# Kernel optimization log

Measured on AMD Instinct MI355X. Metric: run time of the kernel, lower is better.

Reference implementation:

```python
import jax, jax.numpy as jnp
import numpy as np

N = 50000      # nodes
E = 800000     # edges (no self loops; GATConv adds them itself)
F_IN = 128     # in_channels
ED = 16        # edge_attr_dim
H1, C1 = 8, 8  # layer-1 heads/channels -> 64 concat
OUT = 128      # out_channels
G = 256        # graphs in batch
NEG_SLOPE = 0.2


def setup_inputs() -> dict:
    key = jax.random.key(0)
    ks = jax.random.split(key, 20)
    x = jax.random.normal(ks[0], (N, F_IN), jnp.float32)
    src = jax.random.randint(ks[1], (E,), 0, N, jnp.int32)
    off = jax.random.randint(ks[2], (E,), 1, N, jnp.int32)
    dst = ((src + off) % N).astype(jnp.int32)  # guaranteed no self loops
    edge_index = jnp.stack([src, dst])
    edge_attr = jax.random.normal(ks[3], (E, ED), jnp.float32)
    batch = jnp.sort(jax.random.randint(ks[4], (N,), 0, G, jnp.int32))
    def glorot(k, shape, fan_in):
        return jax.random.normal(k, shape, jnp.float32) / np.sqrt(fan_in)
    params = dict(
        W1=glorot(ks[5], (F_IN, H1 * C1), F_IN),
        att_src1=glorot(ks[6], (H1, C1), C1),
        att_dst1=glorot(ks[7], (H1, C1), C1),
        att_edge1=glorot(ks[8], (H1, C1), C1),
        We1=glorot(ks[9], (ED, H1 * C1), ED),
        b1=jnp.zeros((H1 * C1,), jnp.float32),
        W2=glorot(ks[10], (H1 * C1, OUT), H1 * C1),
        att_src2=glorot(ks[11], (1, OUT), OUT),
        att_dst2=glorot(ks[12], (1, OUT), OUT),
        att_edge2=glorot(ks[13], (1, OUT), OUT),
        We2=glorot(ks[14], (ED, OUT), ED),
        b2=jnp.zeros((OUT,), jnp.float32),
    )
    return dict(x=x, edge_index=edge_index, edge_attr=edge_attr, batch=batch, **params)


def _segment_softmax(a, seg, n):
    m = jax.ops.segment_max(a, seg, num_segments=n)
    e = jnp.exp(a - m[seg])
    s = jax.ops.segment_sum(e, seg, num_segments=n)
    return e / (s[seg] + 1e-16)


def _gat_layer(x, src, dst, ea_full, W, a_s, a_d, a_e, We, b, heads, ch, concat):
    n = x.shape[0]
    xw = (x @ W).reshape(n, heads, ch)                       # [N,H,C]
    al_s = jnp.einsum('nhc,hc->nh', xw, a_s)                  # [N,H]
    al_d = jnp.einsum('nhc,hc->nh', xw, a_d)
    ew = (ea_full @ We).reshape(-1, heads, ch)                # [E',H,C]
    al_e = jnp.einsum('ehc,hc->eh', ew, a_e)
    alpha = al_s[src] + al_d[dst] + al_e                      # [E',H]
    alpha = jax.nn.leaky_relu(alpha, NEG_SLOPE)
    alpha = _segment_softmax(alpha, dst, n)                   # softmax over incoming edges
    out = jax.ops.segment_sum(xw[src] * alpha[:, :, None], dst, num_segments=n)
    out = out.reshape(n, heads * ch) if concat else out.mean(axis=1)
    return out + b


def reference(x, edge_index, edge_attr, batch,
              W1, att_src1, att_dst1, att_edge1, We1, b1,
              W2, att_src2, att_dst2, att_edge2, We2, b2):
    src, dst = edge_index[0], edge_index[1]
    n = x.shape[0]
    # add self loops; self-loop edge_attr = mean of incoming edge_attr (fill_value='mean')
    ones = jnp.ones((src.shape[0],), x.dtype)
    deg = jax.ops.segment_sum(ones, dst, num_segments=n)
    ea_self = jax.ops.segment_sum(edge_attr, dst, num_segments=n) / jnp.maximum(deg, 1.0)[:, None]
    loop = jnp.arange(n, dtype=src.dtype)
    src_f = jnp.concatenate([src, loop])
    dst_f = jnp.concatenate([dst, loop])
    ea_full = jnp.concatenate([edge_attr, ea_self], axis=0)

    h = _gat_layer(x, src_f, dst_f, ea_full, W1, att_src1, att_dst1, att_edge1, We1, b1, H1, C1, True)
    h = jax.nn.elu(h)
    h = _gat_layer(h, src_f, dst_f, ea_full, W2, att_src2, att_dst2, att_edge2, We2, b2, 1, OUT, True)

    # global mean pool over graphs
    cnt = jax.ops.segment_sum(jnp.ones((n,), h.dtype), batch, num_segments=G)
    pooled = jax.ops.segment_sum(h, batch, num_segments=G) / jnp.maximum(cnt, 1.0)[:, None]
    return pooled
```

## Files before the change

### kernel.cpp

```cpp
#include <hip/hip_runtime.h>
#include <hip/hip_bf16.h>
#include <math.h>

#define N_NODES 50000
#define N_EDGES 800000
#define F_IN    128
#define ED_DIM  16
#define D1      64
#define NGRAPH  256
#define OUT_C   128

__global__ void prep_kernel(const float* __restrict__ W1, const float* __restrict__ W2,
                            float* __restrict__ W1t, float* __restrict__ W2t) {
  int t = blockIdx.x * 256 + threadIdx.x;
  if (t < 64 * 128) {
    int k = t >> 6, c = t & 63;
    W1t[c * 128 + k] = W1[t];
    int k2 = t >> 7, c2 = t & 127;
    W2t[c2 * 64 + k2] = W2[t];
  }
}

__global__ void hist_kernel(const int* __restrict__ dst, int* __restrict__ deg) {
  int i = blockIdx.x * blockDim.x + threadIdx.x;
  int stride = gridDim.x * blockDim.x;
  for (; i < N_EDGES; i += stride) atomicAdd(&deg[dst[i]], 1);
}

__global__ void scan1_kernel(const int* __restrict__ deg, int* __restrict__ offs,
                             int* __restrict__ bsum) {
  __shared__ int sh[256];
  int b = blockIdx.x, t = threadIdx.x, i = b * 256 + t;
  int v = (i < N_NODES) ? deg[i] : 0;
  sh[t] = v;
  __syncthreads();
  for (int o = 1; o < 256; o <<= 1) {
    int tv = (t >= o) ? sh[t - o] : 0;
    __syncthreads();
    sh[t] += tv;
    __syncthreads();
  }
  if (i < N_NODES) offs[i + 1] = sh[t];
  if (t == 255) bsum[b] = sh[255];
}

__global__ void scan2_kernel(int* __restrict__ bsum) {
  __shared__ int sh[256];
  int t = threadIdx.x;
  sh[t] = (t < 196) ? bsum[t] : 0;
  __syncthreads();
  for (int o = 1; o < 256; o <<= 1) {
    int tv = (t >= o) ? sh[t - o] : 0;
    __syncthreads();
    sh[t] += tv;
    __syncthreads();
  }
  if (t < 196) bsum[t] = (t > 0) ? sh[t - 1] : 0;
}

__global__ void scan3_kernel(const int* __restrict__ bsum, int* __restrict__ offs) {
  int b = blockIdx.x, t = threadIdx.x, i = b * 256 + t;
  if (i < N_NODES) offs[i + 1] += bsum[b];
  if (i == 0) offs[0] = 0;
}

__global__ void scatter_kernel(const int* __restrict__ src, const int* __restrict__ dst,
                               const float* __restrict__ ea,
                               const float* __restrict__ We1, const float* __restrict__ ae1,
                               const float* __restrict__ We2, const float* __restrict__ ae2,
                               const int* __restrict__ offs, int* __restrict__ cnt,
                               float* __restrict__ rec) {
  __shared__ float M1s[16][8];
  __shared__ float M2s[16];
  int t = threadIdx.x;
  if (t < 128) {
    int d = t >> 3, h = t & 7;
    float s = 0.f;
    #pragma unroll
    for (int c = 0; c < 8; ++c) s = fmaf(We1[d * 64 + h * 8 + c], ae1[h * 8 + c], s);
    M1s[d][h] = s;
  } else if (t < 144) {
    int d = t - 128;
    float s = 0.f;
    for (int c = 0; c < 128; ++c) s = fmaf(We2[d * 128 + c], ae2[c], s);
    M2s[d] = s;
  }
  __syncthreads();
  int i = blockIdx.x * blockDim.x + t;
  int stride = gridDim.x * blockDim.x;
  for (; i < N_EDGES; i += stride) {
    int s = src[i], d = dst[i];
    float e[16];
    const float4* ea4 = (const float4*)(ea + (size_t)i * 16);
    #pragma unroll
    for (int q = 0; q < 4; ++q) {
      float4 v = ea4[q];
      e[q * 4] = v.x; e[q * 4 + 1] = v.y; e[q * 4 + 2] = v.z; e[q * 4 + 3] = v.w;
    }
    int pos = offs[d] + atomicAdd(&cnt[d], 1);
    float r[8];
    #pragma unroll
    for (int h = 0; h < 8; ++h) {
      float sacc = 0.f;
      #pragma unroll
      for (int dd = 0; dd < 16; ++dd) sacc = fmaf(e[dd], M1s[dd][h], sacc);
      r[h] = sacc;
    }
    float s2 = 0.f;
    #pragma unroll
    for (int dd = 0; dd < 16; ++dd) s2 = fmaf(e[dd], M2s[dd], s2);
    float4* o4 = (float4*)(rec + (size_t)pos * 16);
    o4[0] = make_float4(__int_as_float(s), r[0], r[1], r[2]);
    o4[1] = make_float4(r[3], r[4], r[5], r[6]);
    o4[2] = make_float4(r[7], s2, 0.f, 0.f);
    o4[3] = make_float4(0.f, 0.f, 0.f, 0.f);
  }
}

__global__ __launch_bounds__(256) void gemm1_kernel(
    const float* __restrict__ x, const float* __restrict__ W1t,
    const float* __restrict__ as1, const float* __restrict__ ad1,
    float* __restrict__ xw1, float* __restrict__ al_s1, float* __restrict__ al_d1) {
  __shared__ float xl[64 * 132];
  __shared__ float wl[64 * 132];
  int t = threadIdx.x;
  int row0 = blockIdx.x * 64;
  const float4* xg = (const float4*)(x + (size_t)row0 * 128);
  const float4* wg = (const float4*)W1t;
  #pragma unroll
  for (int j = 0; j < 8; ++j) {
    int idx = t + j * 256;
    int r = idx >> 5, kq = idx & 31;
    float4 v = make_float4(0.f, 0.f, 0.f, 0.f);
    if (row0 + r < N_NODES) v = xg[r * 32 + kq];
    *(float4*)&xl[r * 132 + kq * 4] = v;
    *(float4*)&wl[(idx >> 5) * 132 + kq * 4] = wg[idx];
  }
  __syncthreads();
  int c0 = t & 15;
  int r4 = (t >> 4) * 4;
  float acc[4][4];
  #pragma unroll
  for (int i = 0; i < 4; ++i)
    #pragma unroll
    for (int j = 0; j < 4; ++j) acc[i][j] = 0.f;
  #pragma unroll 4
  for (int kq = 0; kq < 32; ++kq) {
    float4 xv[4], wv[4];
    #pragma unroll
    for (int i = 0; i < 4; ++i) xv[i] = *(const float4*)&xl[(r4 + i) * 132 + kq * 4];
    #pragma unroll
    for (int j = 0; j < 4; ++j) wv[j] = *(const float4*)&wl[(c0 + 16 * j) * 132 + kq * 4];
    #pragma unroll
    for (int i = 0; i < 4; ++i)
      #pragma unroll
      for (int j = 0; j < 4; ++j) {
        acc[i][j] = fmaf(xv[i].x, wv[j].x, acc[i][j]);
        acc[i][j] = fmaf(xv[i].y, wv[j].y, acc[i][j]);
        acc[i][j] = fmaf(xv[i].z, wv[j].z, acc[i][j]);
        acc[i][j] = fmaf(xv[i].w, wv[j].w, acc[i][j]);
      }
  }
  #pragma unroll
  for (int i = 0; i < 4; ++i) {
    int r = row0 + r4 + i;
    if (r < N_NODES) {
      #pragma unroll
      for (int j = 0; j < 4; ++j) xw1[(size_t)r * 64 + c0 + 16 * j] = acc[i][j];
    }
  }
  float ps[4][4], pd[4][4];
  #pragma unroll
  for (int j = 0; j < 4; ++j) {
    float asv = as1[c0 + 16 * j], adv = ad1[c0 + 16 * j];
    #pragma unroll
    for (int i = 0; i < 4; ++i) { ps[i][j] = acc[i][j] * asv; pd[i][j] = acc[i][j] * adv; }
  }
  #pragma unroll
  for (int m = 1; m <= 4; m <<= 1)
    #pragma unroll
    for (int i = 0; i < 4; ++i)
      #pragma unroll
      for (int j = 0; j < 4; ++j) {
        ps[i][j] += __shfl_xor(ps[i][j], m);
        pd[i][j] += __shfl_xor(pd[i][j], m);
      }
  if ((t & 7) == 0) {
    int half = (c0 >> 3) & 1;
    #pragma unroll
    for (int i = 0; i < 4; ++i) {
      int r = row0 + r4 + i;
      if (r < N_NODES) {
        #pragma unroll
        for (int j = 0; j < 4; ++j) {
          int h = 2 * j + half;
          al_s1[r * 8 + h] = ps[i][j];
          al_d1[r * 8 + h] = pd[i][j];
        }
      }
    }
  }
}

__global__ void agg1_kernel(const int* __restrict__ offs, const float* __restrict__ rec,
                            const float* __restrict__ al_s1, const float* __restrict__ al_d1,
                            const float* __restrict__ xw1,
                            const float* __restrict__ b1, float* __restrict__ h1) {
  int node = blockIdx.x * 4 + (threadIdx.x >> 6);
  if (node >= N_NODES) return;
  int lane = threadIdx.x & 63;
  int h = lane >> 3;
  int base = offs[node], end = offs[node + 1];
  int degn = end - base;
  float adv = al_d1[node * 8 + h];
  float m = -INFINITY, ssum = 0.f, acc = 0.f, sume = 0.f;
  int j = base;
  for (; j + 1 < end; j += 2) {
    const float* r0 = rec + (size_t)j * 16;
    const float* r1 = r0 + 16;
    int s0 = __float_as_int(r0[0]); float ae0 = r0[1 + h];
    int s1 = __float_as_int(r1[0]); float ae1 = r1[1 + h];
    float x0 = xw1[(size_t)s0 * 64 + lane];
    float x1 = xw1[(size_t)s1 * 64 + lane];
    float a0 = al_s1[s0 * 8 + h] + adv + ae0;
    float a1 = al_s1[s1 * 8 + h] + adv + ae1;
    sume += ae0 + ae1;
    a0 = (a0 > 0.f) ? a0 : 0.2f * a0;
    a1 = (a1 > 0.f) ? a1 : 0.2f * a1;
    float nm = fmaxf(m, fmaxf(a0, a1));
    float sc = __expf(m - nm), e0 = __expf(a0 - nm), e1 = __expf(a1 - nm);
    ssum = ssum * sc + e0 + e1;
    acc = acc * sc + e0 * x0 + e1 * x1;
    m = nm;
  }
  if (j < end) {
    const float* r0 = rec + (size_t)j * 16;
    int s0 = __float_as_int(r0[0]); float ae0 = r0[1 + h];
    float x0 = xw1[(size_t)s0 * 64 + lane];
    float a0 = al_s1[s0 * 8 + h] + adv + ae0;
    sume += ae0;
    a0 = (a0 > 0.f) ? a0 : 0.2f * a0;
    float nm = fmaxf(m, a0);
    float sc = __expf(m - nm), e0 = __expf(a0 - nm);
    ssum = ssum * sc + e0;
    acc = acc * sc + e0 * x0;
    m = nm;
  }
  float aes = sume / (float)max(degn, 1);
  float a = al_s1[node * 8 + h] + adv + aes;
  a = (a > 0.f) ? a : 0.2f * a;
  float nm = fmaxf(m, a);
  float sc = __expf(m - nm);
  float e = __expf(a - nm);
  ssum = ssum * sc + e;
  acc = acc * sc + e * xw1[(size_t)node * 64 + lane];
  float o = acc / (ssum + 1e-16f) + b1[lane];
  h1[(size_t)node * 64 + lane] = (o > 0.f) ? o : expm1f(o);
}

__global__ __launch_bounds__(256) void gemm2_kernel(
    const float* __restrict__ h1, const float* __restrict__ W2t,
    const float* __restrict__ as2, const float* __restrict__ ad2,
    float* __restrict__ xw2, float* __restrict__ al_s2, float* __restrict__ al_d2) {
  __shared__ float hl[64 * 68];
  __shared__ float wl[128 * 68];
  int t = threadIdx.x;
  int row0 = blockIdx.x * 64;
  const float4* hg = (const float4*)(h1 + (size_t)row0 * 64);
  const float4* wg = (const float4*)W2t;
  #pragma unroll
  for (int j = 0; j < 4; ++j) {
    int idx = t + j * 256;
    int r = idx >> 4, kq = idx & 15;
    float4 v = make_float4(0.f, 0.f, 0.f, 0.f);
    if (row0 + r < N_NODES) v = hg[r * 16 + kq];
    *(float4*)&hl[r * 68 + kq * 4] = v;
  }
  #pragma unroll
  for (int j = 0; j < 8; ++j) {
    int idx = t + j * 256;
    int c = idx >> 4, kq = idx & 15;
    *(float4*)&wl[c * 68 + kq * 4] = wg[idx];
  }
  __syncthreads();
  int c0 = t & 31;
  int r8 = (t >> 5) * 8;
  float acc[8][4];
  #pragma unroll
  for (int i = 0; i < 8; ++i)
    #pragma unroll
    for (int j = 0; j < 4; ++j) acc[i][j] = 0.f;
  #pragma unroll 2
  for (int kq = 0; kq < 16; ++kq) {
    float4 xv[8], wv[4];
    #pragma unroll
    for (int i = 0; i < 8; ++i) xv[i] = *(const float4*)&hl[(r8 + i) * 68 + kq * 4];
    #pragma unroll
    for (int j = 0; j < 4; ++j) wv[j] = *(const float4*)&wl[(c0 + 32 * j) * 68 + kq * 4];
    #pragma unroll
    for (int i = 0; i < 8; ++i)
      #pragma unroll
      for (int j = 0; j < 4; ++j) {
        acc[i][j] = fmaf(xv[i].x, wv[j].x, acc[i][j]);
        acc[i][j] = fmaf(xv[i].y, wv[j].y, acc[i][j]);
        acc[i][j] = fmaf(xv[i].z, wv[j].z, acc[i][j]);
        acc[i][j] = fmaf(xv[i].w, wv[j].w, acc[i][j]);
      }
  }
  #pragma unroll
  for (int i = 0; i < 8; ++i) {
    int r = row0 + r8 + i;
    if (r < N_NODES) {
      #pragma unroll
      for (int j = 0; j < 4; ++j) xw2[(size_t)r * 128 + c0 + 32 * j] = acc[i][j];
    }
  }
  float ps[8], pd[8];
  #pragma unroll
  for (int i = 0; i < 8; ++i) { ps[i] = 0.f; pd[i] = 0.f; }
  #pragma unroll
  for (int j = 0; j < 4; ++j) {
    float asv = as2[c0 + 32 * j], adv = ad2[c0 + 32 * j];
    #pragma unroll
    for (int i = 0; i < 8; ++i) { ps[i] = fmaf(acc[i][j], asv, ps[i]); pd[i] = fmaf(acc[i][j], adv, pd[i]); }
  }
  #pragma unroll
  for (int m = 1; m <= 16; m <<= 1)
    #pragma unroll
    for (int i = 0; i < 8; ++i) {
      ps[i] += __shfl_xor(ps[i], m);
      pd[i] += __shfl_xor(pd[i], m);
    }
  if (c0 == 0) {
    #pragma unroll
    for (int i = 0; i < 8; ++i) {
      int r = row0 + r8 + i;
      if (r < N_NODES) { al_s2[r] = ps[i]; al_d2[r] = pd[i]; }
    }
  }
}

__global__ void agg2_kernel(const int* __restrict__ offs, const float* __restrict__ rec,
                            const float* __restrict__ al_s2, const float* __restrict__ al_d2,
                            const float* __restrict__ xw2,
                            const float* __restrict__ b2, float* __restrict__ h2) {
  int node = blockIdx.x * 4 + (threadIdx.x >> 6);
  if (node >= N_NODES) return;
  int lane = threadIdx.x & 63;
  int base = offs[node], end = offs[node + 1];
  int degn = end - base;
  float adv = al_d2[node];
  float m = -INFINITY, ssum = 0.f, acc0 = 0.f, acc1 = 0.f, sume = 0.f;
  int j = base;
  for (; j + 1 < end; j += 2) {
    const float* r0 = rec + (size_t)j * 16;
    const float* r1 = r0 + 16;
    int s0 = __float_as_int(r0[0]); float ae0 = r0[9];
    int s1 = __float_as_int(r1[0]); float ae1 = r1[9];
    float x0a = xw2[(size_t)s0 * 128 + lane];
    float x0b = xw2[(size_t)s0 * 128 + 64 + lane];
    float x1a = xw2[(size_t)s1 * 128 + lane];
    float x1b = xw2[(size_t)s1 * 128 + 64 + lane];
    float a0 = al_s2[s0] + adv + ae0;
    float a1 = al_s2[s1] + adv + ae1;
    sume += ae0 + ae1;
    a0 = (a0 > 0.f) ? a0 : 0.2f * a0;
    a1 = (a1 > 0.f) ? a1 : 0.2f * a1;
    float nm = fmaxf(m, fmaxf(a0, a1));
    float sc = __expf(m - nm), e0 = __expf(a0 - nm), e1 = __expf(a1 - nm);
    ssum = ssum * sc + e0 + e1;
    acc0 = acc0 * sc + e0 * x0a + e1 * x1a;
    acc1 = acc1 * sc + e0 * x0b + e1 * x1b;
    m = nm;
  }
  if (j < end) {
    const float* r0 = rec + (size_t)j * 16;
    int s0 = __float_as_int(r0[0]); float ae0 = r0[9];
    float x0a = xw2[(size_t)s0 * 128 + lane];
    float x0b = xw2[(size_t)s0 * 128 + 64 + lane];
    float a0 = al_s2[s0] + adv + ae0;
    sume += ae0;
    a0 = (a0 > 0.f) ? a0 : 0.2f * a0;
    float nm = fmaxf(m, a0);
    float sc = __expf(m - nm), e0 = __expf(a0 - nm);
    ssum = ssum * sc + e0;
    acc0 = acc0 * sc + e0 * x0a;
    acc1 = acc1 * sc + e0 * x0b;
    m = nm;
  }
  float aes = sume / (float)max(degn, 1);
  float a = al_s2[node] + adv + aes;
  a = (a > 0.f) ? a : 0.2f * a;
  float nm = fmaxf(m, a);
  float sc = __expf(m - nm);
  float e = __expf(a - nm);
  ssum = ssum * sc + e;
  acc0 = acc0 * sc + e * xw2[(size_t)node * 128 + lane];
  acc1 = acc1 * sc + e * xw2[(size_t)node * 128 + 64 + lane];
  float inv = 1.f / (ssum + 1e-16f);
  h2[(size_t)node * 128 + lane] = acc0 * inv + b2[lane];
  h2[(size_t)node * 128 + 64 + lane] = acc1 * inv + b2[lane + 64];
}

__global__ void gstart_kernel(const int* __restrict__ batch, int* __restrict__ gstart) {
  int n = blockIdx.x * blockDim.x + threadIdx.x;
  if (n >= N_NODES) return;
  int b = batch[n];
  if (n == 0) {
    for (int g = 0; g <= b; ++g) gstart[g] = 0;
  } else {
    int pb = batch[n - 1];
    for (int g = pb + 1; g <= b; ++g) gstart[g] = n;
  }
  if (n == N_NODES - 1) {
    for (int g = b + 1; g <= NGRAPH; ++g) gstart[g] = N_NODES;
  }
}

__global__ void pool_kernel(const float* __restrict__ h2, const int* __restrict__ gstart,
                            float* __restrict__ out) {
  int g = blockIdx.x;
  int c = threadIdx.x;
  int s0 = gstart[g], s1 = gstart[g + 1];
  float s = 0.f;
  for (int r = s0; r < s1; ++r) s += h2[(size_t)r * 128 + c];
  out[g * 128 + c] = s / fmaxf((float)(s1 - s0), 1.f);
}

extern "C" void kernel_launch(void* const* d_in, const int* in_sizes, int n_in,
                              void* d_out, int out_size, void* d_ws, size_t ws_size,
                              hipStream_t stream) {
  const float* x      = (const float*)d_in[0];
  const int*   eidx   = (const int*)d_in[1];
  const float* ea     = (const float*)d_in[2];
  const int*   batch  = (const int*)d_in[3];
  const float* W1     = (const float*)d_in[4];
  const float* as1    = (const float*)d_in[5];
  const float* ad1    = (const float*)d_in[6];
  const float* ae1    = (const float*)d_in[7];
  const float* We1    = (const float*)d_in[8];
  const float* b1     = (const float*)d_in[9];
  const float* W2     = (const float*)d_in[10];
  const float* as2    = (const float*)d_in[11];
  const float* ad2    = (const float*)d_in[12];
  const float* ae2    = (const float*)d_in[13];
  const float* We2    = (const float*)d_in[14];
  const float* b2     = (const float*)d_in[15];
  float* out = (float*)d_out;

  const int* src = eidx;
  const int* dst = eidx + N_EDGES;

  char* base = (char*)d_ws;
  size_t o = 0;
  #define ALLOC(name, bytes) size_t name = o; o += (((size_t)(bytes)) + 255) & ~(size_t)255;
  ALLOC(o_degcnt, 2 * N_NODES * 4)
  ALLOC(o_offs,   (N_NODES + 1) * 4)
  ALLOC(o_bsum,   256 * 4)
  ALLOC(o_rec,    (size_t)N_EDGES * 16 * 4)
  ALLOC(o_w1t,    64 * 128 * 4)
  ALLOC(o_w2t,    128 * 64 * 4)
  ALLOC(o_xw1,    (size_t)N_NODES * 64 * 4)
  ALLOC(o_als1,   N_NODES * 8 * 4)
  ALLOC(o_ald1,   N_NODES * 8 * 4)
  ALLOC(o_h1,     (size_t)N_NODES * 64 * 4)
  ALLOC(o_xw2,    (size_t)N_NODES * 128 * 4)
  ALLOC(o_als2,   N_NODES * 4)
  ALLOC(o_ald2,   N_NODES * 4)
  ALLOC(o_gs,     (NGRAPH + 1) * 4)
  #undef ALLOC

  int*   deg     = (int*)(base + o_degcnt);
  int*   cnt     = deg + N_NODES;
  int*   offs    = (int*)(base + o_offs);
  int*   bsum    = (int*)(base + o_bsum);
  float* rec     = (float*)(base + o_rec);
  float* W1t     = (float*)(base + o_w1t);
  float* W2t     = (float*)(base + o_w2t);
  float* xw1     = (float*)(base + o_xw1);
  float* al_s1   = (float*)(base + o_als1);
  float* al_d1   = (float*)(base + o_ald1);
  float* h1      = (float*)(base + o_h1);
  float* xw2     = (float*)(base + o_xw2);
  float* al_s2   = (float*)(base + o_als2);
  float* al_d2   = (float*)(base + o_ald2);
  float* h2      = (float*)(base + o_xw1);
  int*   gstart  = (int*)(base + o_gs);

  hipMemsetAsync(deg, 0, (size_t)2 * N_NODES * 4, stream);

  prep_kernel<<<32, 256, 0, stream>>>(W1, W2, W1t, W2t);
  hist_kernel<<<1024, 256, 0, stream>>>(dst, deg);
  scan1_kernel<<<196, 256, 0, stream>>>(deg, offs, bsum);
  scan2_kernel<<<1, 256, 0, stream>>>(bsum);
  scan3_kernel<<<196, 256, 0, stream>>>(bsum, offs);
  scatter_kernel<<<2048, 256, 0, stream>>>(src, dst, ea, We1, ae1, We2, ae2,
                                           offs, cnt, rec);
  gemm1_kernel<<<(N_NODES + 63) / 64, 256, 0, stream>>>(x, W1t, as1, ad1, xw1, al_s1, al_d1);
  agg1_kernel<<<(N_NODES + 3) / 4, 256, 0, stream>>>(offs, rec, al_s1, al_d1, xw1, b1, h1);
  gemm2_kernel<<<(N_NODES + 63) / 64, 256, 0, stream>>>(h1, W2t, as2, ad2, xw2, al_s2, al_d2);
  agg2_kernel<<<(N_NODES + 3) / 4, 256, 0, stream>>>(offs, rec, al_s2, al_d2, xw2, b2, h2);
  gstart_kernel<<<(N_NODES + 255) / 256, 256, 0, stream>>>(batch, gstart);
  pool_kernel<<<NGRAPH, 128, 0, stream>>>(h2, gstart, out);
}
```

Baseline: 512.9 us.

## Compute edge attention logits in histogram pass and shrink CSR scatter to int2

Moves the per-edge attention-logit projection out of the scatter kernel into the degree-histogram pass, writing the results in original edge order to separate arrays. The scatter kernel now writes only an 8-byte (src, edge id) pair per edge instead of a 64-byte padded record, so the random-position scatter writes far less data. In exchange, the aggregation kernels do an extra indirect gather into the logit arrays through the edge id, which loses the contiguous per-node record reads.

```diff
diff --git a/kernel.cpp b/kernel.cpp
--- a/kernel.cpp
+++ b/kernel.cpp
@@ -21,10 +21,54 @@
   }
 }
 
-__global__ void hist_kernel(const int* __restrict__ dst, int* __restrict__ deg) {
-  int i = blockIdx.x * blockDim.x + threadIdx.x;
+__global__ void histcalc_kernel(const int* __restrict__ dst, const float* __restrict__ ea,
+                                const float* __restrict__ We1, const float* __restrict__ ae1w,
+                                const float* __restrict__ We2, const float* __restrict__ ae2w,
+                                int* __restrict__ deg,
+                                float* __restrict__ ale1, float* __restrict__ ale2) {
+  __shared__ float M1s[16][8];
+  __shared__ float M2s[16];
+  int t = threadIdx.x;
+  if (t < 128) {
+    int d = t >> 3, h = t & 7;
+    float s = 0.f;
+    #pragma unroll
+    for (int c = 0; c < 8; ++c) s = fmaf(We1[d * 64 + h * 8 + c], ae1w[h * 8 + c], s);
+    M1s[d][h] = s;
+  } else if (t < 144) {
+    int d = t - 128;
+    float s = 0.f;
+    for (int c = 0; c < 128; ++c) s = fmaf(We2[d * 128 + c], ae2w[c], s);
+    M2s[d] = s;
+  }
+  __syncthreads();
+  int i = blockIdx.x * blockDim.x + t;
   int stride = gridDim.x * blockDim.x;
-  for (; i < N_EDGES; i += stride) atomicAdd(&deg[dst[i]], 1);
+  for (; i < N_EDGES; i += stride) {
+    atomicAdd(&deg[dst[i]], 1);
+    float e[16];
+    const float4* ea4 = (const float4*)(ea + (size_t)i * 16);
+    #pragma unroll
+    for (int q = 0; q < 4; ++q) {
+      float4 v = ea4[q];
+      e[q * 4] = v.x; e[q * 4 + 1] = v.y; e[q * 4 + 2] = v.z; e[q * 4 + 3] = v.w;
+    }
+    float r[8];
+    #pragma unroll
+    for (int h = 0; h < 8; ++h) {
+      float sacc = 0.f;
+      #pragma unroll
+      for (int dd = 0; dd < 16; ++dd) sacc = fmaf(e[dd], M1s[dd][h], sacc);
+      r[h] = sacc;
+    }
+    float s2 = 0.f;
+    #pragma unroll
+    for (int dd = 0; dd < 16; ++dd) s2 = fmaf(e[dd], M2s[dd], s2);
+    float4* o4 = (float4*)(ale1 + (size_t)i * 8);
+    o4[0] = make_float4(r[0], r[1], r[2], r[3]);
+    o4[1] = make_float4(r[4], r[5], r[6], r[7]);
+    ale2[i] = s2;
+  }
 }
 
 __global__ void scan1_kernel(const int* __restrict__ deg, int* __restrict__ offs,
@@ -65,55 +109,14 @@
 }
 
 __global__ void scatter_kernel(const int* __restrict__ src, const int* __restrict__ dst,
-                               const float* __restrict__ ea,
-                               const float* __restrict__ We1, const float* __restrict__ ae1,
-                               const float* __restrict__ We2, const float* __restrict__ ae2,
                                const int* __restrict__ offs, int* __restrict__ cnt,
-                               float* __restrict__ rec) {
-  __shared__ float M1s[16][8];
-  __shared__ float M2s[16];
-  int t = threadIdx.x;
-  if (t < 128) {
-    int d = t >> 3, h = t & 7;
-    float s = 0.f;
-    #pragma unroll
-    for (int c = 0; c < 8; ++c) s = fmaf(We1[d * 64 + h * 8 + c], ae1[h * 8 + c], s);
-    M1s[d][h] = s;
-  } else if (t < 144) {
-    int d = t - 128;
-    float s = 0.f;
-    for (int c = 0; c < 128; ++c) s = fmaf(We2[d * 128 + c], ae2[c], s);
-    M2s[d] = s;
-  }
-  __syncthreads();
-  int i = blockIdx.x * blockDim.x + t;
+                               int2* __restrict__ csr) {
+  int i = blockIdx.x * blockDim.x + threadIdx.x;
   int stride = gridDim.x * blockDim.x;
   for (; i < N_EDGES; i += stride) {
-    int s = src[i], d = dst[i];
-    float e[16];
-    const float4* ea4 = (const float4*)(ea + (size_t)i * 16);
-    #pragma unroll
-    for (int q = 0; q < 4; ++q) {
-      float4 v = ea4[q];
-      e[q * 4] = v.x; e[q * 4 + 1] = v.y; e[q * 4 + 2] = v.z; e[q * 4 + 3] = v.w;
-    }
+    int d = dst[i];
     int pos = offs[d] + atomicAdd(&cnt[d], 1);
-    float r[8];
-    #pragma unroll
-    for (int h = 0; h < 8; ++h) {
-      float sacc = 0.f;
-      #pragma unroll
-      for (int dd = 0; dd < 16; ++dd) sacc = fmaf(e[dd], M1s[dd][h], sacc);
-      r[h] = sacc;
-    }
-    float s2 = 0.f;
-    #pragma unroll
-    for (int dd = 0; dd < 16; ++dd) s2 = fmaf(e[dd], M2s[dd], s2);
-    float4* o4 = (float4*)(rec + (size_t)pos * 16);
-    o4[0] = make_float4(__int_as_float(s), r[0], r[1], r[2]);
-    o4[1] = make_float4(r[3], r[4], r[5], r[6]);
-    o4[2] = make_float4(r[7], s2, 0.f, 0.f);
-    o4[3] = make_float4(0.f, 0.f, 0.f, 0.f);
+    csr[pos] = make_int2(src[i], i);
   }
 }
 
@@ -202,7 +205,8 @@
   }
 }
 
-__global__ void agg1_kernel(const int* __restrict__ offs, const float* __restrict__ rec,
+__global__ void agg1_kernel(const int* __restrict__ offs, const int2* __restrict__ csr,
+                            const float* __restrict__ ale1,
                             const float* __restrict__ al_s1, const float* __restrict__ al_d1,
                             const float* __restrict__ xw1,
                             const float* __restrict__ b1, float* __restrict__ h1) {
@@ -216,14 +220,13 @@
   float m = -INFINITY, ssum = 0.f, acc = 0.f, sume = 0.f;
   int j = base;
   for (; j + 1 < end; j += 2) {
-    const float* r0 = rec + (size_t)j * 16;
-    const float* r1 = r0 + 16;
-    int s0 = __float_as_int(r0[0]); float ae0 = r0[1 + h];
-    int s1 = __float_as_int(r1[0]); float ae1 = r1[1 + h];
-    float x0 = xw1[(size_t)s0 * 64 + lane];
-    float x1 = xw1[(size_t)s1 * 64 + lane];
-    float a0 = al_s1[s0 * 8 + h] + adv + ae0;
-    float a1 = al_s1[s1 * 8 + h] + adv + ae1;
+    int2 c0v = csr[j], c1v = csr[j + 1];
+    float ae0 = ale1[(size_t)c0v.y * 8 + h];
+    float ae1 = ale1[(size_t)c1v.y * 8 + h];
+    float x0 = xw1[(size_t)c0v.x * 64 + lane];
+    float x1 = xw1[(size_t)c1v.x * 64 + lane];
+    float a0 = al_s1[c0v.x * 8 + h] + adv + ae0;
+    float a1 = al_s1[c1v.x * 8 + h] + adv + ae1;
     sume += ae0 + ae1;
     a0 = (a0 > 0.f) ? a0 : 0.2f * a0;
     a1 = (a1 > 0.f) ? a1 : 0.2f * a1;
@@ -234,10 +237,10 @@
     m = nm;
   }
   if (j < end) {
-    const float* r0 = rec + (size_t)j * 16;
-    int s0 = __float_as_int(r0[0]); float ae0 = r0[1 + h];
-    float x0 = xw1[(size_t)s0 * 64 + lane];
-    float a0 = al_s1[s0 * 8 + h] + adv + ae0;
+    int2 c0v = csr[j];
+    float ae0 = ale1[(size_t)c0v.y * 8 + h];
+    float x0 = xw1[(size_t)c0v.x * 64 + lane];
+    float a0 = al_s1[c0v.x * 8 + h] + adv + ae0;
     sume += ae0;
     a0 = (a0 > 0.f) ? a0 : 0.2f * a0;
     float nm = fmaxf(m, a0);
@@ -340,7 +343,8 @@
   }
 }
 
-__global__ void agg2_kernel(const int* __restrict__ offs, const float* __restrict__ rec,
+__global__ void agg2_kernel(const int* __restrict__ offs, const int2* __restrict__ csr,
+                            const float* __restrict__ ale2,
                             const float* __restrict__ al_s2, const float* __restrict__ al_d2,
                             const float* __restrict__ xw2,
                             const float* __restrict__ b2, float* __restrict__ h2) {
@@ -353,16 +357,15 @@
   float m = -INFINITY, ssum = 0.f, acc0 = 0.f, acc1 = 0.f, sume = 0.f;
   int j = base;
   for (; j + 1 < end; j += 2) {
-    const float* r0 = rec + (size_t)j * 16;
-    const float* r1 = r0 + 16;
-    int s0 = __float_as_int(r0[0]); float ae0 = r0[9];
-    int s1 = __float_as_int(r1[0]); float ae1 = r1[9];
-    float x0a = xw2[(size_t)s0 * 128 + lane];
-    float x0b = xw2[(size_t)s0 * 128 + 64 + lane];
-    float x1a = xw2[(size_t)s1 * 128 + lane];
-    float x1b = xw2[(size_t)s1 * 128 + 64 + lane];
-    float a0 = al_s2[s0] + adv + ae0;
-    float a1 = al_s2[s1] + adv + ae1;
+    int2 c0v = csr[j], c1v = csr[j + 1];
+    float ae0 = ale2[c0v.y];
+    float ae1 = ale2[c1v.y];
+    float x0a = xw2[(size_t)c0v.x * 128 + lane];
+    float x0b = xw2[(size_t)c0v.x * 128 + 64 + lane];
+    float x1a = xw2[(size_t)c1v.x * 128 + lane];
+    float x1b = xw2[(size_t)c1v.x * 128 + 64 + lane];
+    float a0 = al_s2[c0v.x] + adv + ae0;
+    float a1 = al_s2[c1v.x] + adv + ae1;
     sume += ae0 + ae1;
     a0 = (a0 > 0.f) ? a0 : 0.2f * a0;
     a1 = (a1 > 0.f) ? a1 : 0.2f * a1;
@@ -374,11 +377,11 @@
     m = nm;
   }
   if (j < end) {
-    const float* r0 = rec + (size_t)j * 16;
-    int s0 = __float_as_int(r0[0]); float ae0 = r0[9];
-    float x0a = xw2[(size_t)s0 * 128 + lane];
-    float x0b = xw2[(size_t)s0 * 128 + 64 + lane];
-    float a0 = al_s2[s0] + adv + ae0;
+    int2 c0v = csr[j];
+    float ae0 = ale2[c0v.y];
+    float x0a = xw2[(size_t)c0v.x * 128 + lane];
+    float x0b = xw2[(size_t)c0v.x * 128 + 64 + lane];
+    float a0 = al_s2[c0v.x] + adv + ae0;
     sume += ae0;
     a0 = (a0 > 0.f) ? a0 : 0.2f * a0;
     float nm = fmaxf(m, a0);
@@ -457,7 +460,9 @@
   ALLOC(o_degcnt, 2 * N_NODES * 4)
   ALLOC(o_offs,   (N_NODES + 1) * 4)
   ALLOC(o_bsum,   256 * 4)
-  ALLOC(o_rec,    (size_t)N_EDGES * 16 * 4)
+  ALLOC(o_csr,    (size_t)N_EDGES * 8)
+  ALLOC(o_ale1,   (size_t)N_EDGES * 8 * 4)
+  ALLOC(o_ale2,   (size_t)N_EDGES * 4)
   ALLOC(o_w1t,    64 * 128 * 4)
   ALLOC(o_w2t,    128 * 64 * 4)
   ALLOC(o_xw1,    (size_t)N_NODES * 64 * 4)
@@ -474,7 +479,9 @@
   int*   cnt     = deg + N_NODES;
   int*   offs    = (int*)(base + o_offs);
   int*   bsum    = (int*)(base + o_bsum);
-  float* rec     = (float*)(base + o_rec);
+  int2*  csr     = (int2*)(base + o_csr);
+  float* ale1    = (float*)(base + o_ale1);
+  float* ale2    = (float*)(base + o_ale2);
   float* W1t     = (float*)(base + o_w1t);
   float* W2t     = (float*)(base + o_w2t);
   float* xw1     = (float*)(base + o_xw1);
@@ -490,16 +497,15 @@
   hipMemsetAsync(deg, 0, (size_t)2 * N_NODES * 4, stream);
 
   prep_kernel<<<32, 256, 0, stream>>>(W1, W2, W1t, W2t);
-  hist_kernel<<<1024, 256, 0, stream>>>(dst, deg);
+  histcalc_kernel<<<1024, 256, 0, stream>>>(dst, ea, We1, ae1, We2, ae2, deg, ale1, ale2);
   scan1_kernel<<<196, 256, 0, stream>>>(deg, offs, bsum);
   scan2_kernel<<<1, 256, 0, stream>>>(bsum);
   scan3_kernel<<<196, 256, 0, stream>>>(bsum, offs);
-  scatter_kernel<<<2048, 256, 0, stream>>>(src, dst, ea, We1, ae1, We2, ae2,
-                                           offs, cnt, rec);
+  scatter_kernel<<<1024, 256, 0, stream>>>(src, dst, offs, cnt, csr);
   gemm1_kernel<<<(N_NODES + 63) / 64, 256, 0, stream>>>(x, W1t, as1, ad1, xw1, al_s1, al_d1);
-  agg1_kernel<<<(N_NODES + 3) / 4, 256, 0, stream>>>(offs, rec, al_s1, al_d1, xw1, b1, h1);
+  agg1_kernel<<<(N_NODES + 3) / 4, 256, 0, stream>>>(offs, csr, ale1, al_s1, al_d1, xw1, b1, h1);
   gemm2_kernel<<<(N_NODES + 63) / 64, 256, 0, stream>>>(h1, W2t, as2, ad2, xw2, al_s2, al_d2);
-  agg2_kernel<<<(N_NODES + 3) / 4, 256, 0, stream>>>(offs, rec, al_s2, al_d2, xw2, b2, h2);
+  agg2_kernel<<<(N_NODES + 3) / 4, 256, 0, stream>>>(offs, csr, ale2, al_s2, al_d2, xw2, b2, h2);
   gstart_kernel<<<(N_NODES + 255) / 256, 256, 0, stream>>>(batch, gstart);
   pool_kernel<<<NGRAPH, 128, 0, stream>>>(h2, gstart, out);
 }
```

After: 487.1 us. 5.0% less time.
